# Performance work log

Hardware: AMD Instinct MI355X
Metric: run time of the kernel (lower is better)

The kernel has to match this reference:

```python
import jax, jax.numpy as jnp
import numpy as np

B, T, E, H = 2, 2048, 768, 12
HD = E // H  # 64


def setup_inputs() -> dict:
    key = jax.random.key(0)
    ks = jax.random.split(key, 5)
    s = 0.02
    return {
        "token_embeddings": jax.random.normal(ks[0], (B, T, E), dtype=jnp.float32),
        "W_Q": jax.random.normal(ks[1], (E, E), dtype=jnp.float32) * s,
        "W_K": jax.random.normal(ks[2], (E, E), dtype=jnp.float32) * s,
        "W_V": jax.random.normal(ks[3], (E, E), dtype=jnp.float32) * s,
        "W_pool": jax.random.normal(ks[4], (E, E), dtype=jnp.float32) * s,
    }


def reference(token_embeddings, W_Q, W_K, W_V, W_pool):
    # torch Linear (bias=False): y = x @ W.T with W of shape (out, in)
    Q = token_embeddings @ W_Q.T
    K = token_embeddings @ W_K.T
    V = token_embeddings @ W_V.T
    # Faithful replication of the module's unusual head split:
    # contiguous view (B, T, E) -> (B, H, T, HD), NOT the standard split+transpose.
    Q = Q.reshape(B, H, T, HD)
    K = K.reshape(B, H, T, HD)
    V = V.reshape(B, H, T, HD)
    scores = jnp.einsum("bhqd,bhkd->bhqk", Q, K)  # [B,H,T,T]
    causal = jnp.tril(jnp.ones((T, T), dtype=bool))
    scores = jnp.where(causal, scores, -jnp.inf)
    attn = jax.nn.softmax(scores / jnp.float32(np.sqrt(HD)), axis=-1)
    out = jnp.einsum("bhqk,bhkd->bhqd", attn, V)  # [B,H,T,HD]
    # Faithful: transpose(1,2) then contiguous view back to (B, T, E)
    out = jnp.transpose(out, (0, 2, 1, 3)).reshape(B, T, E)
    return out @ W_pool.T
```

## Files before the change

### kernel.cpp

```cpp
#include <hip/hip_runtime.h>

typedef unsigned short u16;
typedef unsigned int u32;
typedef __attribute__((ext_vector_type(8))) short bf16x8;
typedef __attribute__((ext_vector_type(4))) short bf16x4;
typedef __attribute__((ext_vector_type(4))) float f32x4;
typedef __attribute__((ext_vector_type(4))) unsigned short u16x4;
typedef __attribute__((ext_vector_type(2))) unsigned int u32x2;

#define GM 4096
#define GN 768
#define GK 768
#define QSCALE 0.18033688011112042f

#define HAS_MFMA16 __has_builtin(__builtin_amdgcn_mfma_f32_16x16x16bf16_1k)

static __device__ __forceinline__ u16 f2bf(float f) {
  union { float f; unsigned u; } v; v.f = f;
  unsigned u = v.u;
  return (u16)((u + 0x7FFFu + ((u >> 16) & 1u)) >> 16);
}

static __device__ __forceinline__ float exp2_hw(float x) {
  float r;
  asm("v_exp_f32 %0, %1" : "=v"(r) : "v"(x));
  return r;
}

static __device__ __forceinline__ u32 pack_rn(float lo, float hi) {
  u32 a = __float_as_uint(lo) + 0x8000u;
  u32 b = __float_as_uint(hi) + 0x8000u;
  return (a >> 16) | (b & 0xFFFF0000u);
}

static __device__ __forceinline__ void gld16(const void* g, void* l) {
  __builtin_amdgcn_global_load_lds((__attribute__((address_space(1))) void*)(g),
                                   (__attribute__((address_space(3))) void*)(l),
                                   16, 0, 0);
}

__global__ void cvt_bf16(const float* __restrict__ in, u16* __restrict__ out, int n4) {
  int i = blockIdx.x * blockDim.x + threadIdx.x;
  if (i < n4) {
    float4 v = ((const float4*)in)[i];
    u16x4 o;
    o[0] = f2bf(v.x); o[1] = f2bf(v.y); o[2] = f2bf(v.z); o[3] = f2bf(v.w);
    ((u16x4*)out)[i] = o;
  }
}

__global__ void cvt_w4(const float* __restrict__ w0, const float* __restrict__ w1,
                       const float* __restrict__ w2, const float* __restrict__ w3,
                       u16* __restrict__ o0, u16* __restrict__ o1,
                       u16* __restrict__ o2, u16* __restrict__ o3, int n4) {
  const float* in = blockIdx.y == 0 ? w0 : (blockIdx.y == 1 ? w1 : (blockIdx.y == 2 ? w2 : w3));
  u16* out = blockIdx.y == 0 ? o0 : (blockIdx.y == 1 ? o1 : (blockIdx.y == 2 ? o2 : o3));
  int i = blockIdx.x * blockDim.x + threadIdx.x;
  if (i < n4) {
    float4 v = ((const float4*)in)[i];
    u16x4 o;
    o[0] = f2bf(v.x); o[1] = f2bf(v.y); o[2] = f2bf(v.z); o[3] = f2bf(v.w);
    ((u16x4*)out)[i] = o;
  }
}

template<int F32OUT>
static __device__ __forceinline__ void gemm_core(const u16* __restrict__ A,
                                                 const u16* __restrict__ B,
                                                 void* __restrict__ O,
                                                 u16* lA, u16* lB, float scale)
{
  const int tid = threadIdx.x;
  const int wave = tid >> 6, lane = tid & 63;
  const int g = lane >> 4, c = lane & 15;
  const int wr = (wave >> 1) * 64, wc = (wave & 1) * 64;
  const int tm = blockIdx.x * 128, tn = blockIdx.y * 128;

  f32x4 acc[4][4] = {};

  const int srow = lane >> 2;
  const int scolb = (lane & 3) * 16;
  const char* gA = (const char*)(A + (size_t)tm * GK);
  const char* gB = (const char*)(B + (size_t)tn * GK);

  for (int k0 = 0; k0 < GK; k0 += 32) {
#pragma unroll
    for (int i = 0; i < 2; ++i) {
      const int chunk = wave * 2 + i;
      const int row = chunk * 16 + srow;
      gld16(gA + (size_t)row * (GK * 2) + k0 * 2 + scolb, (char*)lA + chunk * 1024);
      gld16(gB + (size_t)row * (GK * 2) + k0 * 2 + scolb, (char*)lB + chunk * 1024);
    }
    __syncthreads();
    bf16x8 af[4], bfr[4];
#pragma unroll
    for (int m = 0; m < 4; ++m)
      af[m] = *(const bf16x8*)((const char*)lA + (wr + m * 16 + c) * 64 + g * 16);
#pragma unroll
    for (int n = 0; n < 4; ++n)
      bfr[n] = *(const bf16x8*)((const char*)lB + (wc + n * 16 + c) * 64 + g * 16);
#pragma unroll
    for (int m = 0; m < 4; ++m)
#pragma unroll
      for (int n = 0; n < 4; ++n)
        acc[m][n] = __builtin_amdgcn_mfma_f32_16x16x32_bf16(af[m], bfr[n], acc[m][n], 0, 0, 0);
    __syncthreads();
  }

#pragma unroll
  for (int m = 0; m < 4; ++m)
#pragma unroll
    for (int n = 0; n < 4; ++n) {
      const int row0 = tm + wr + m * 16 + g * 4;
      const int col = tn + wc + n * 16 + c;
#pragma unroll
      for (int r = 0; r < 4; ++r) {
        if (F32OUT)
          ((float*)O)[(size_t)(row0 + r) * GN + col] = acc[m][n][r];
        else
          ((u16*)O)[(size_t)(row0 + r) * GN + col] = f2bf(acc[m][n][r] * scale);
      }
    }
}

__global__ __launch_bounds__(256) void gemm_qkv(const u16* __restrict__ A,
    const u16* __restrict__ B0, const u16* __restrict__ B1, const u16* __restrict__ B2,
    u16* __restrict__ O0, u16* __restrict__ O1, u16* __restrict__ O2)
{
  __shared__ u16 lA[4096], lB[4096];
  const u16* B = blockIdx.z == 0 ? B0 : (blockIdx.z == 1 ? B1 : B2);
  u16* O = blockIdx.z == 0 ? O0 : (blockIdx.z == 1 ? O1 : O2);
  const float scale = blockIdx.z == 0 ? QSCALE : 1.0f;
  gemm_core<0>(A, B, O, lA, lB, scale);
}

__global__ __launch_bounds__(256) void gemm_pool(const u16* __restrict__ A,
    const u16* __restrict__ B, float* __restrict__ O)
{
  __shared__ u16 lA[4096], lB[4096];
  gemm_core<1>(A, B, O, lA, lB, 1.0f);
}

__global__ __launch_bounds__(256) void vtrans(const u16* __restrict__ V, u16* __restrict__ VT) {
  const int tblk = blockIdx.x;
  const int bh = blockIdx.y;
  __shared__ u16 tile[64][72];
  const u16* Vh = V + (size_t)bh * 131072;
  u16* Vt = VT + (size_t)bh * 131072;
  const int tid = threadIdx.x;
  const int t0 = tblk * 64;
#pragma unroll
  for (int i = 0; i < 4; ++i) {
    int idx = i * 256 + tid;
    int row = idx >> 4;
    int c4 = idx & 15;
    u16x4 v = *(const u16x4*)(Vh + (size_t)(t0 + row) * 64 + c4 * 4);
    tile[row][c4 * 4 + 0] = v[0]; tile[row][c4 * 4 + 1] = v[1];
    tile[row][c4 * 4 + 2] = v[2]; tile[row][c4 * 4 + 3] = v[3];
  }
  __syncthreads();
#pragma unroll
  for (int i = 0; i < 4; ++i) {
    int idx = i * 256 + tid;
    int d = idx >> 4;
    int t4 = idx & 15;
    u16x4 o;
    o[0] = tile[t4 * 4 + 0][d]; o[1] = tile[t4 * 4 + 1][d];
    o[2] = tile[t4 * 4 + 2][d]; o[3] = tile[t4 * 4 + 3][d];
    *(u16x4*)(Vt + (size_t)d * 2048 + t0 + t4 * 4) = o;
  }
}

static __device__ __forceinline__ void stage_tile(const char* gbase, int rowstride,
                                                  char* lbuf, int wave, int lane) {
#pragma unroll
  for (int i = 0; i < 2; ++i) {
    const int chunk = i * 256 + wave * 64 + lane;
    const int row = chunk >> 3;
    const int colb = (chunk & 7) << 4;
    const char* src = gbase + (size_t)row * rowstride + (colb ^ ((row & 7) << 4));
    char* dst = lbuf + i * 4096 + wave * 1024;
    gld16(src, dst);
  }
}

__global__ __launch_bounds__(256) void attn(const u16* __restrict__ Q,
                                            const u16* __restrict__ Km,
                                            const u16* __restrict__ VT,
                                            u16* __restrict__ X2)
{
  const int qblk = blockIdx.x;
  const int bh = blockIdx.y;
  const int b = bh / 12, h = bh % 12;
  const int tid = threadIdx.x, wave = tid >> 6, lane = tid & 63;
  const int g = lane >> 4, c = lane & 15;
  const int swr = (c & 7) << 4;
  const int swz = ((c & 7) ^ (c >> 3)) << 4;

  __shared__ char Kl[2][8192];
  __shared__ char Vl[2][8192];
#if !HAS_MFMA16
  __shared__ u16 Plds[4][1024];
  u16* pl = Plds[wave];
#endif
  (void)swz;

  const char* Khb = (const char*)(Km + (size_t)bh * 131072);
  const char* Vhb = (const char*)(VT + (size_t)bh * 131072);
  const u16* Qh = Q + (size_t)bh * 131072;

  const int q0 = qblk * 64 + wave * 16;
  const int nkt = qblk + 1;

  stage_tile(Khb, 128, Kl[0], wave, lane);
  stage_tile(Vhb, 4096, Vl[0], wave, lane);

  bf16x8 qf[2];
#pragma unroll
  for (int kk = 0; kk < 2; ++kk)
    qf[kk] = *(const bf16x8*)(Qh + (size_t)(q0 + c) * 64 + kk * 32 + g * 8);

  f32x4 oacc[4] = {};
  float lsum = 0.f;

  __syncthreads();

  for (int kt = 0; kt < nkt; ++kt) {
    const int cur = kt & 1;
    if (kt + 1 < nkt) {
      stage_tile(Khb + (size_t)(kt + 1) * 8192, 128, Kl[cur ^ 1], wave, lane);
      stage_tile(Vhb + (size_t)(kt + 1) * 128, 4096, Vl[cur ^ 1], wave, lane);
    }
    f32x4 s[4] = {};
    __builtin_amdgcn_s_setprio(1);
#pragma unroll
    for (int kk = 0; kk < 2; ++kk)
#pragma unroll
      for (int n = 0; n < 4; ++n) {
        bf16x8 kf = *(const bf16x8*)(Kl[cur] + (size_t)(n * 16 + c) * 128 + ((kk * 64 + g * 16) ^ swr));
        s[n] = __builtin_amdgcn_mfma_f32_16x16x32_bf16(kf, qf[kk], s[n], 0, 0, 0);
      }
    __builtin_amdgcn_s_setprio(0);

#if HAS_MFMA16
    bf16x4 pa[4];
    if (kt == nkt - 1) {
      const int qrow = q0 + c;
#pragma unroll
      for (int n = 0; n < 4; ++n) {
        const int k0i = kt * 64 + n * 16 + g * 4;
        float p0 = (k0i + 0 > qrow) ? 0.f : exp2_hw(s[n][0]);
        float p1 = (k0i + 1 > qrow) ? 0.f : exp2_hw(s[n][1]);
        float p2 = (k0i + 2 > qrow) ? 0.f : exp2_hw(s[n][2]);
        float p3 = (k0i + 3 > qrow) ? 0.f : exp2_hw(s[n][3]);
        lsum += (p0 + p1) + (p2 + p3);
        u32x2 pw; pw[0] = pack_rn(p0, p1); pw[1] = pack_rn(p2, p3);
        pa[n] = __builtin_bit_cast(bf16x4, pw);
      }
    } else {
#pragma unroll
      for (int n = 0; n < 4; ++n) {
        float p0 = exp2_hw(s[n][0]);
        float p1 = exp2_hw(s[n][1]);
        float p2 = exp2_hw(s[n][2]);
        float p3 = exp2_hw(s[n][3]);
        lsum += (p0 + p1) + (p2 + p3);
        u32x2 pw; pw[0] = pack_rn(p0, p1); pw[1] = pack_rn(p2, p3);
        pa[n] = __builtin_bit_cast(bf16x4, pw);
      }
    }
    __builtin_amdgcn_s_setprio(1);
#pragma unroll
    for (int n = 0; n < 4; ++n)
#pragma unroll
      for (int nn = 0; nn < 4; ++nn) {
        bf16x4 vb = *(const bf16x4*)(Vl[cur] + (size_t)(nn * 16 + c) * 128 + ((n * 32 + g * 8) ^ swr));
        oacc[nn] = __builtin_amdgcn_mfma_f32_16x16x16bf16_1k(pa[n], vb, oacc[nn], 0, 0, 0);
      }
    __builtin_amdgcn_s_setprio(0);
#else
    if (kt == nkt - 1) {
      const int qrow = q0 + c;
#pragma unroll
      for (int n = 0; n < 4; ++n) {
        const int k0i = kt * 64 + n * 16 + g * 4;
        float p0 = (k0i + 0 > qrow) ? 0.f : exp2_hw(s[n][0]);
        float p1 = (k0i + 1 > qrow) ? 0.f : exp2_hw(s[n][1]);
        float p2 = (k0i + 2 > qrow) ? 0.f : exp2_hw(s[n][2]);
        float p3 = (k0i + 3 > qrow) ? 0.f : exp2_hw(s[n][3]);
        lsum += (p0 + p1) + (p2 + p3);
        u32x2 pw; pw[0] = pack_rn(p0, p1); pw[1] = pack_rn(p2, p3);
        *(u32x2*)((char*)pl + c * 128 + ((n * 32 + g * 8) ^ swz)) = pw;
      }
    } else {
#pragma unroll
      for (int n = 0; n < 4; ++n) {
        float p0 = exp2_hw(s[n][0]);
        float p1 = exp2_hw(s[n][1]);
        float p2 = exp2_hw(s[n][2]);
        float p3 = exp2_hw(s[n][3]);
        lsum += (p0 + p1) + (p2 + p3);
        u32x2 pw; pw[0] = pack_rn(p0, p1); pw[1] = pack_rn(p2, p3);
        *(u32x2*)((char*)pl + c * 128 + ((n * 32 + g * 8) ^ swz)) = pw;
      }
    }
    __builtin_amdgcn_s_setprio(1);
#pragma unroll
    for (int kk = 0; kk < 2; ++kk) {
      bf16x8 pab = *(const bf16x8*)((const char*)pl + c * 128 + ((kk * 64 + g * 16) ^ swz));
#pragma unroll
      for (int n = 0; n < 4; ++n) {
        bf16x8 vfb = *(const bf16x8*)(Vl[cur] + (size_t)(n * 16 + c) * 128 + ((kk * 64 + g * 16) ^ swr));
        oacc[n] = __builtin_amdgcn_mfma_f32_16x16x32_bf16(pab, vfb, oacc[n], 0, 0, 0);
      }
    }
    __builtin_amdgcn_s_setprio(0);
#endif
    __syncthreads();
  }

  float tot = lsum;
  tot += __shfl_xor(tot, 16);
  tot += __shfl_xor(tot, 32);
  float linv[4];
#pragma unroll
  for (int r = 0; r < 4; ++r)
    linv[r] = __frcp_rn(__shfl(tot, g * 4 + r));
#pragma unroll
  for (int n = 0; n < 4; ++n)
#pragma unroll
    for (int r = 0; r < 4; ++r) {
      const float o = oacc[n][r] * linv[r];
      const int t = q0 + g * 4 + r;
      X2[((size_t)b * 2048 + t) * 768 + h * 64 + n * 16 + c] = f2bf(o);
    }
}

extern "C" void kernel_launch(void* const* d_in, const int* in_sizes, int n_in,
                              void* d_out, int out_size, void* d_ws, size_t ws_size,
                              hipStream_t stream) {
  const float* x  = (const float*)d_in[0];
  const float* wq = (const float*)d_in[1];
  const float* wk = (const float*)d_in[2];
  const float* wv = (const float*)d_in[3];
  const float* wp = (const float*)d_in[4];

  const size_t SZ_X = (size_t)GM * GN * 2;
  const size_t SZ_W = (size_t)GK * GN * 2;
  char* ws = (char*)d_ws;
  u16* xbf  = (u16*)(ws);
  u16* wqb  = (u16*)(ws + SZ_X);
  u16* wkb  = (u16*)(ws + SZ_X + SZ_W);
  u16* wvb  = (u16*)(ws + SZ_X + 2 * SZ_W);
  u16* wpb  = (u16*)(ws + SZ_X + 3 * SZ_W);
  u16* Qb   = (u16*)(ws + SZ_X + 4 * SZ_W);
  u16* Kb   = (u16*)(ws + 2 * SZ_X + 4 * SZ_W);
  u16* Vb   = (u16*)(ws + 3 * SZ_X + 4 * SZ_W);
  u16* VT   = (u16*)(ws + 4 * SZ_X + 4 * SZ_W);
  u16* X2   = (u16*)(ws + 5 * SZ_X + 4 * SZ_W);
  if (ws_size < 6 * SZ_X + 4 * SZ_W) return;

  cvt_bf16<<<dim3(3072), dim3(256), 0, stream>>>(x, xbf, GM * GN / 4);
  cvt_w4<<<dim3(576, 4), dim3(256), 0, stream>>>(wq, wk, wv, wp, wqb, wkb, wvb, wpb, GK * GN / 4);

  gemm_qkv<<<dim3(32, 6, 3), dim3(256), 0, stream>>>(xbf, wqb, wkb, wvb, Qb, Kb, Vb);
  vtrans<<<dim3(32, 24), dim3(256), 0, stream>>>(Vb, VT);
  attn<<<dim3(32, 24), dim3(256), 0, stream>>>(Qb, Kb, VT, X2);
  gemm_pool<<<dim3(32, 6), dim3(256), 0, stream>>>(X2, wpb, (float*)d_out);
}
```

Before: 105.3 us.

## Fuse V transpose into QKV GEMM epilogue and merge conversion kernels

The V projection GEMM now writes its output straight into the transposed per-head layout that attention consumes, so the separate vtrans kernel and the intermediate V buffer go away. The two fp32-to-bf16 conversion kernels are merged into one launch. Together these drop two kernel launches and one round trip of V through memory. The cost is that the fused epilogue does scattered 2-byte stores with a large stride, which may coalesce poorly.

New measurement: 116.6 us. +10.7%, slower.

```diff
diff --git a/kernel.cpp b/kernel.cpp
--- a/kernel.cpp
+++ b/kernel.cpp
@@ -39,32 +39,29 @@
                                    16, 0, 0);
 }
 
-__global__ void cvt_bf16(const float* __restrict__ in, u16* __restrict__ out, int n4) {
-  int i = blockIdx.x * blockDim.x + threadIdx.x;
-  if (i < n4) {
-    float4 v = ((const float4*)in)[i];
-    u16x4 o;
-    o[0] = f2bf(v.x); o[1] = f2bf(v.y); o[2] = f2bf(v.z); o[3] = f2bf(v.w);
-    ((u16x4*)out)[i] = o;
+__global__ void cvt_all(const float* __restrict__ x,
+                        const float* __restrict__ w0, const float* __restrict__ w1,
+                        const float* __restrict__ w2, const float* __restrict__ w3,
+                        u16* __restrict__ xo,
+                        u16* __restrict__ o0, u16* __restrict__ o1,
+                        u16* __restrict__ o2, u16* __restrict__ o3) {
+  int blk = blockIdx.x;
+  const float* in; u16* out; int base;
+  if (blk < 3072) { in = x; out = xo; base = 0; }
+  else {
+    int wsel = (blk - 3072) / 576;
+    base = 3072 + wsel * 576;
+    in = wsel == 0 ? w0 : (wsel == 1 ? w1 : (wsel == 2 ? w2 : w3));
+    out = wsel == 0 ? o0 : (wsel == 1 ? o1 : (wsel == 2 ? o2 : o3));
   }
-}
-
-__global__ void cvt_w4(const float* __restrict__ w0, const float* __restrict__ w1,
-                       const float* __restrict__ w2, const float* __restrict__ w3,
-                       u16* __restrict__ o0, u16* __restrict__ o1,
-                       u16* __restrict__ o2, u16* __restrict__ o3, int n4) {
-  const float* in = blockIdx.y == 0 ? w0 : (blockIdx.y == 1 ? w1 : (blockIdx.y == 2 ? w2 : w3));
-  u16* out = blockIdx.y == 0 ? o0 : (blockIdx.y == 1 ? o1 : (blockIdx.y == 2 ? o2 : o3));
-  int i = blockIdx.x * blockDim.x + threadIdx.x;
-  if (i < n4) {
-    float4 v = ((const float4*)in)[i];
-    u16x4 o;
-    o[0] = f2bf(v.x); o[1] = f2bf(v.y); o[2] = f2bf(v.z); o[3] = f2bf(v.w);
-    ((u16x4*)out)[i] = o;
-  }
-}
-
-template<int F32OUT>
+  int i = (blk - base) * 256 + threadIdx.x;
+  float4 v = ((const float4*)in)[i];
+  u16x4 o;
+  o[0] = f2bf(v.x); o[1] = f2bf(v.y); o[2] = f2bf(v.z); o[3] = f2bf(v.w);
+  ((u16x4*)out)[i] = o;
+}
+
+template<int MODE>
 static __device__ __forceinline__ void gemm_core(const u16* __restrict__ A,
                                                  const u16* __restrict__ B,
                                                  void* __restrict__ O,
@@ -113,25 +110,35 @@
     for (int n = 0; n < 4; ++n) {
       const int row0 = tm + wr + m * 16 + g * 4;
       const int col = tn + wc + n * 16 + c;
-#pragma unroll
-      for (int r = 0; r < 4; ++r) {
-        if (F32OUT)
-          ((float*)O)[(size_t)(row0 + r) * GN + col] = acc[m][n][r];
-        else
-          ((u16*)O)[(size_t)(row0 + r) * GN + col] = f2bf(acc[m][n][r] * scale);
+      if (MODE == 2) {
+        const int d = col & 63;
+        const int cq = col >> 6;
+#pragma unroll
+        for (int r = 0; r < 4; ++r) {
+          const int u = (row0 + r) * 12 + cq;
+          ((u16*)O)[(size_t)(u >> 11) * 131072 + (size_t)d * 2048 + (u & 2047)] =
+              f2bf(acc[m][n][r]);
+        }
+      } else {
+#pragma unroll
+        for (int r = 0; r < 4; ++r) {
+          if (MODE == 1)
+            ((float*)O)[(size_t)(row0 + r) * GN + col] = acc[m][n][r];
+          else
+            ((u16*)O)[(size_t)(row0 + r) * GN + col] = f2bf(acc[m][n][r] * scale);
+        }
       }
     }
 }
 
 __global__ __launch_bounds__(256) void gemm_qkv(const u16* __restrict__ A,
     const u16* __restrict__ B0, const u16* __restrict__ B1, const u16* __restrict__ B2,
-    u16* __restrict__ O0, u16* __restrict__ O1, u16* __restrict__ O2)
+    u16* __restrict__ O0, u16* __restrict__ O1, u16* __restrict__ VT)
 {
   __shared__ u16 lA[4096], lB[4096];
-  const u16* B = blockIdx.z == 0 ? B0 : (blockIdx.z == 1 ? B1 : B2);
-  u16* O = blockIdx.z == 0 ? O0 : (blockIdx.z == 1 ? O1 : O2);
-  const float scale = blockIdx.z == 0 ? QSCALE : 1.0f;
-  gemm_core<0>(A, B, O, lA, lB, scale);
+  if (blockIdx.z == 0)      gemm_core<0>(A, B0, O0, lA, lB, QSCALE);
+  else if (blockIdx.z == 1) gemm_core<0>(A, B1, O1, lA, lB, 1.0f);
+  else                      gemm_core<2>(A, B2, VT, lA, lB, 1.0f);
 }
 
 __global__ __launch_bounds__(256) void gemm_pool(const u16* __restrict__ A,
@@ -139,36 +146,6 @@
 {
   __shared__ u16 lA[4096], lB[4096];
   gemm_core<1>(A, B, O, lA, lB, 1.0f);
-}
-
-__global__ __launch_bounds__(256) void vtrans(const u16* __restrict__ V, u16* __restrict__ VT) {
-  const int tblk = blockIdx.x;
-  const int bh = blockIdx.y;
-  __shared__ u16 tile[64][72];
-  const u16* Vh = V + (size_t)bh * 131072;
-  u16* Vt = VT + (size_t)bh * 131072;
-  const int tid = threadIdx.x;
-  const int t0 = tblk * 64;
-#pragma unroll
-  for (int i = 0; i < 4; ++i) {
-    int idx = i * 256 + tid;
-    int row = idx >> 4;
-    int c4 = idx & 15;
-    u16x4 v = *(const u16x4*)(Vh + (size_t)(t0 + row) * 64 + c4 * 4);
-    tile[row][c4 * 4 + 0] = v[0]; tile[row][c4 * 4 + 1] = v[1];
-    tile[row][c4 * 4 + 2] = v[2]; tile[row][c4 * 4 + 3] = v[3];
-  }
-  __syncthreads();
-#pragma unroll
-  for (int i = 0; i < 4; ++i) {
-    int idx = i * 256 + tid;
-    int d = idx >> 4;
-    int t4 = idx & 15;
-    u16x4 o;
-    o[0] = tile[t4 * 4 + 0][d]; o[1] = tile[t4 * 4 + 1][d];
-    o[2] = tile[t4 * 4 + 2][d]; o[3] = tile[t4 * 4 + 3][d];
-    *(u16x4*)(Vt + (size_t)d * 2048 + t0 + t4 * 4) = o;
-  }
 }
 
 static __device__ __forceinline__ void stage_tile(const char* gbase, int rowstride,
@@ -355,16 +332,13 @@
   u16* wpb  = (u16*)(ws + SZ_X + 3 * SZ_W);
   u16* Qb   = (u16*)(ws + SZ_X + 4 * SZ_W);
   u16* Kb   = (u16*)(ws + 2 * SZ_X + 4 * SZ_W);
-  u16* Vb   = (u16*)(ws + 3 * SZ_X + 4 * SZ_W);
-  u16* VT   = (u16*)(ws + 4 * SZ_X + 4 * SZ_W);
-  u16* X2   = (u16*)(ws + 5 * SZ_X + 4 * SZ_W);
-  if (ws_size < 6 * SZ_X + 4 * SZ_W) return;
-
-  cvt_bf16<<<dim3(3072), dim3(256), 0, stream>>>(x, xbf, GM * GN / 4);
-  cvt_w4<<<dim3(576, 4), dim3(256), 0, stream>>>(wq, wk, wv, wp, wqb, wkb, wvb, wpb, GK * GN / 4);
-
-  gemm_qkv<<<dim3(32, 6, 3), dim3(256), 0, stream>>>(xbf, wqb, wkb, wvb, Qb, Kb, Vb);
-  vtrans<<<dim3(32, 24), dim3(256), 0, stream>>>(Vb, VT);
+  u16* VT   = (u16*)(ws + 3 * SZ_X + 4 * SZ_W);
+  u16* X2   = (u16*)(ws + 4 * SZ_X + 4 * SZ_W);
+  if (ws_size < 5 * SZ_X + 4 * SZ_W) return;
+
+  cvt_all<<<dim3(3072 + 4 * 576), dim3(256), 0, stream>>>(x, wq, wk, wv, wp,
+                                                          xbf, wqb, wkb, wvb, wpb);
+  gemm_qkv<<<dim3(32, 6, 3), dim3(256), 0, stream>>>(xbf, wqb, wkb, wvb, Qb, Kb, VT);
   attn<<<dim3(32, 24), dim3(256), 0, stream>>>(Qb, Kb, VT, X2);
   gemm_pool<<<dim3(32, 6), dim3(256), 0, stream>>>(X2, wpb, (float*)d_out);
 }
```
